# Kernel optimization log

Measured on AMD Instinct MI355X. Metric: run time of the kernel, lower is better.

Reference implementation:

```python
import jax, jax.numpy as jnp
import numpy as np

B, T, C = 4, 2048, 1024
N_HEAD = 16
HEAD_DIM = C // N_HEAD


def setup_inputs() -> dict:
    key = jax.random.key(0)
    k1, k2, k3 = jax.random.split(key, 3)
    x = jax.random.normal(k1, (B, T, C), dtype=jnp.float32)
    # torch Linear(n_embd, 3*n_embd, bias=False): weight [out,in]; store transposed [in,out]
    w_qkv = jax.random.normal(k2, (C, 3 * C), dtype=jnp.float32) * (1.0 / np.sqrt(C))
    w_proj = jax.random.normal(k3, (C, C), dtype=jnp.float32) * (1.0 / np.sqrt(C))
    return {"x": x, "w_qkv": w_qkv, "w_proj": w_proj}


def reference(x, w_qkv, w_proj):
    Bb, Tt, Cc = x.shape
    qkv = x @ w_qkv  # [B,T,3C]
    q, k, v = jnp.split(qkv, 3, axis=2)
    # [B,T,H,D] -> [B,H,T,D]
    def heads(t):
        return t.reshape(Bb, Tt, N_HEAD, HEAD_DIM).transpose(0, 2, 1, 3)
    q, k, v = heads(q), heads(k), heads(v)
    att = jnp.einsum("bhqd,bhkd->bhqk", q, k) / jnp.sqrt(jnp.float32(HEAD_DIM))
    causal = jnp.tril(jnp.ones((Tt, Tt), dtype=bool))
    att = jnp.where(causal, att, -jnp.inf)
    att = jax.nn.softmax(att, axis=-1)
    y = jnp.einsum("bhqk,bhkd->bhqd", att, v)  # [B,H,T,D]
    y = y.transpose(0, 2, 1, 3).reshape(Bb, Tt, Cc)
    return y @ w_proj
```

## Files before the change

kernel.cpp:

```cpp
#include <hip/hip_runtime.h>
#include <hip/hip_bf16.h>

typedef unsigned short u16;
typedef __bf16 bf16x8 __attribute__((ext_vector_type(8)));
typedef float f32x4 __attribute__((ext_vector_type(4)));
typedef float f32x16 __attribute__((ext_vector_type(16)));
typedef unsigned short u16x8 __attribute__((ext_vector_type(8)));
typedef unsigned short u16x4 __attribute__((ext_vector_type(4)));
typedef unsigned int u32x4 __attribute__((ext_vector_type(4)));

__device__ __forceinline__ u16 f2bf(float f) {
  unsigned u = __builtin_bit_cast(unsigned, f);
  u += 0x7FFFu + ((u >> 16) & 1u);
  return (u16)(u >> 16);
}

__device__ __forceinline__ unsigned cvt_pk_bf16(float lo, float hi_) {
  unsigned r;
  asm("v_cvt_pk_bf16_f32 %0, %1, %2" : "=v"(r) : "v"(lo), "v"(hi_));
  return r;
}

#define GLD16(gp, lp)                                                          \
  __builtin_amdgcn_global_load_lds(                                            \
      (const __attribute__((address_space(1))) void*)(gp),                     \
      (__attribute__((address_space(3))) void*)(lp), 16, 0, 0)


__global__ __launch_bounds__(256) void cast_f32_bf16(
    const float* __restrict__ in, u16* __restrict__ out, int n4) {
  int i = blockIdx.x * 256 + threadIdx.x;
  if (i >= n4) return;
  float4 v = ((const float4*)in)[i];
  u16x4 o = {f2bf(v.x), f2bf(v.y), f2bf(v.z), f2bf(v.w)};
  *(u16x4*)(out + (size_t)i * 4) = o;
}

__global__ __launch_bounds__(256) void transpose_cast(
    const float* __restrict__ in, u16* __restrict__ out, int R, int C) {
  __shared__ float t[32][33];
  int c0 = blockIdx.x * 32, r0 = blockIdx.y * 32;
  int tx = threadIdx.x, ty = threadIdx.y;
#pragma unroll
  for (int k = 0; k < 4; ++k)
    t[ty + 8 * k][tx] = in[(size_t)(r0 + ty + 8 * k) * C + c0 + tx];
  __syncthreads();
#pragma unroll
  for (int k = 0; k < 4; ++k)
    out[(size_t)(c0 + ty + 8 * k) * R + r0 + tx] = f2bf(t[tx][ty + 8 * k]);
}


template <int EPI>
__global__ __launch_bounds__(256) void gemm_bt(
    const u16* __restrict__ A, const u16* __restrict__ Bt, int K,
    u16* __restrict__ Qd, u16* __restrict__ Kd, u16* __restrict__ Vd,
    float* __restrict__ Od, int N) {
  __shared__ u16 As[128 * 64];
  __shared__ u16 Bs[128 * 64];
  int tid = threadIdx.x;
  int l = tid & 63, w = tid >> 6;
  int wr = w >> 1, wc = w & 1;
  int lr = l & 15, lg = l >> 4;
  int m0 = blockIdx.y * 128, n0 = blockIdx.x * 128;

  f32x4 acc[4][4];
  f32x4 z4 = {0.f, 0.f, 0.f, 0.f};
#pragma unroll
  for (int mi = 0; mi < 4; ++mi)
#pragma unroll
    for (int ni = 0; ni < 4; ++ni) acc[mi][ni] = z4;

  for (int kt = 0; kt < K; kt += 64) {
#pragma unroll
    for (int it = 0; it < 4; ++it) {
      int q = it * 256 + tid;
      int r = q >> 3, s = q & 7;
      int sw = (s ^ (r & 7)) << 3;
      GLD16(A + (size_t)(m0 + r) * K + kt + sw, As + it * 2048 + w * 512);
      GLD16(Bt + (size_t)(n0 + r) * K + kt + sw, Bs + it * 2048 + w * 512);
    }
    __syncthreads();

#pragma unroll
    for (int ks2 = 0; ks2 < 2; ++ks2) {
      bf16x8 af[4], bfv[4];
#pragma unroll
      for (int mi = 0; mi < 4; ++mi) {
        int row = wr * 64 + mi * 16 + lr;
        af[mi] = *(const bf16x8*)&As[row * 64 + (((ks2 * 4 + lg) ^ (row & 7)) << 3)];
      }
#pragma unroll
      for (int ni = 0; ni < 4; ++ni) {
        int col = wc * 64 + ni * 16 + lr;
        bfv[ni] = *(const bf16x8*)&Bs[col * 64 + (((ks2 * 4 + lg) ^ (col & 7)) << 3)];
      }
#pragma unroll
      for (int mi = 0; mi < 4; ++mi)
#pragma unroll
        for (int ni = 0; ni < 4; ++ni)
          acc[mi][ni] = __builtin_amdgcn_mfma_f32_16x16x32_bf16(
              af[mi], bfv[ni], acc[mi][ni], 0, 0, 0);
    }
    __syncthreads();
  }

  if (EPI == 0) {
    int s_blk = n0 >> 10;
    u16* dst = (s_blk == 0) ? Qd : ((s_blk == 1) ? Kd : Vd);
#pragma unroll
    for (int mi = 0; mi < 4; ++mi)
#pragma unroll
      for (int ni = 0; ni < 4; ++ni)
#pragma unroll
        for (int i = 0; i < 4; ++i) {
          int m = m0 + wr * 64 + mi * 16 + lg * 4 + i;
          int n = n0 + wc * 64 + ni * 16 + lr;
          int b = m >> 11, t = m & 2047;
          int c = n & 1023, h = c >> 6, d = c & 63;
          dst[((size_t)(b * 16 + h) * 2048 + t) * 64 + d] = f2bf(acc[mi][ni][i]);
        }
  } else {
#pragma unroll
    for (int mi = 0; mi < 4; ++mi)
#pragma unroll
      for (int ni = 0; ni < 4; ++ni)
#pragma unroll
        for (int i = 0; i < 4; ++i) {
          int m = m0 + wr * 64 + mi * 16 + lg * 4 + i;
          int n = n0 + wc * 64 + ni * 16 + lr;
          Od[(size_t)m * N + n] = acc[mi][ni][i];
        }
  }
}


__global__ __launch_bounds__(256, 2) void attn_fwd(
    const u16* __restrict__ Qg, const u16* __restrict__ Kg,
    const u16* __restrict__ Vg, u16* __restrict__ Yg) {
  __shared__ u16 Ks[2][64 * 64];
  __shared__ u16 Vt[64 * 64];

  int tid = threadIdx.x;
  int l = tid & 63, w = tid >> 6;
  int l31 = l & 31, hi = l >> 5, l7 = l & 7;
  int bid = blockIdx.x;
  int pp = bid >> 6;
  int bh = bid & 63;
  const u16* Qb = Qg + (size_t)bh * 131072;
  const u16* Kb = Kg + (size_t)bh * 131072;
  const u16* Vb = Vg + (size_t)bh * 131072;
  int b = bh >> 4, h = bh & 15;

  int vtr = tid >> 3, vdq = tid & 7;

#pragma unroll 1
  for (int ph = 0; ph < 2; ++ph) {
    int qt = ph ? (15 - pp) : pp;
    int q0w = qt * 128 + w * 32;
    int jn = 2 * qt + 1;

    bf16x8 qreg[4];
#pragma unroll
    for (int ds = 0; ds < 4; ++ds)
      qreg[ds] =
          *(const bf16x8*)(Qb + (size_t)(q0w + l31) * 64 + ds * 16 + hi * 8);

    f32x16 o_acc[2];
#pragma unroll
    for (int dt = 0; dt < 2; ++dt)
#pragma unroll
      for (int r = 0; r < 16; ++r) o_acc[dt][r] = 0.f;
    float m_run = -3e38f, l_run = 0.f;

    u16x8 va, vb;
#pragma unroll
    for (int it = 0; it < 2; ++it) {
      int r = (it * 256 + tid) >> 3;
      GLD16(Kb + (size_t)r * 64 + (((tid & 7) ^ (r & 7)) << 3),
            &Ks[0][it * 2048 + w * 512]);
    }
    va = *(const u16x8*)(Vb + (size_t)(2 * vtr) * 64 + vdq * 8);
    vb = *(const u16x8*)(Vb + (size_t)(2 * vtr + 1) * 64 + vdq * 8);

    for (int j = 0; j <= jn; ++j) {
      int kv0 = j * 64;
      const u16* ksb = Ks[j & 1];
#pragma unroll
      for (int jj = 0; jj < 8; ++jj) {
        int d = vdq * 8 + jj;
        unsigned wv = (unsigned)va[jj] | ((unsigned)vb[jj] << 16);
        *(unsigned*)(Vt + d * 64 + (((vtr >> 2) ^ jj ^ vdq) << 3) +
                     ((vtr & 3) << 1)) = wv;
      }
      __syncthreads();

      if (j < jn) {
        int kv1 = kv0 + 64;
#pragma unroll
        for (int it = 0; it < 2; ++it) {
          int r = (it * 256 + tid) >> 3;
          GLD16(Kb + (size_t)(kv1 + r) * 64 + (((tid & 7) ^ (r & 7)) << 3),
                &Ks[(j + 1) & 1][it * 2048 + w * 512]);
        }
        va = *(const u16x8*)(Vb + (size_t)(kv1 + 2 * vtr) * 64 + vdq * 8);
        vb = *(const u16x8*)(Vb + (size_t)(kv1 + 2 * vtr + 1) * 64 + vdq * 8);
      }

      bool active = kv0 <= q0w + 31;
      if (active) {
        int qg = q0w + l31;
        bf16x8 kf[2][4];
#pragma unroll
        for (int kt = 0; kt < 2; ++kt)
#pragma unroll
          for (int ds = 0; ds < 4; ++ds)
            kf[kt][ds] = *(const bf16x8*)&ksb[(32 * kt + l31) * 64 +
                                              (((2 * ds + hi) ^ l7) << 3)];
        f32x16 sa[2];
        __builtin_amdgcn_s_setprio(1);
#pragma unroll
        for (int kt = 0; kt < 2; ++kt) {
          f32x16 acc;
#pragma unroll
          for (int r = 0; r < 16; ++r) acc[r] = 0.f;
#pragma unroll
          for (int ds = 0; ds < 4; ++ds)
            acc = __builtin_amdgcn_mfma_f32_32x32x16_bf16(kf[kt][ds], qreg[ds],
                                                          acc, 0, 0, 0);
          sa[kt] = acc;
        }
        __builtin_amdgcn_s_setprio(0);

        float mloc = -3e38f;
        if (kv0 + 63 > q0w) {
#pragma unroll
          for (int kt = 0; kt < 2; ++kt)
#pragma unroll
            for (int r = 0; r < 16; ++r) {
              int kg = kv0 + kt * 32 + ((r & 3) + 8 * (r >> 2) + 4 * hi);
              float v = sa[kt][r];
              v = (kg <= qg) ? v : -8e30f;
              sa[kt][r] = v;
              mloc = fmaxf(mloc, v);
            }
        } else {
#pragma unroll
          for (int kt = 0; kt < 2; ++kt)
#pragma unroll
            for (int r = 0; r < 16; ++r) mloc = fmaxf(mloc, sa[kt][r]);
        }
        float mx = fmaxf(mloc, __shfl_xor(mloc, 32)) * 0.125f;
        if (!__all(mx <= m_run + 8.f)) {
          float mn = fmaxf(m_run, mx);
          float fsc = __expf(m_run - mn);
          m_run = mn;
          l_run *= fsc;
#pragma unroll
          for (int r = 0; r < 16; ++r) {
            float fv = __shfl(fsc, (r & 3) + 8 * (r >> 2) + 4 * hi + 32 * hi);
            o_acc[0][r] *= fv;
            o_acc[1][r] *= fv;
          }
        }
        float mm = m_run * 1.44269504f;
        float lloc = 0.f;
#pragma unroll
        for (int kt = 0; kt < 2; ++kt)
#pragma unroll
          for (int r = 0; r < 16; ++r) {
            float p = exp2f(__builtin_fmaf(sa[kt][r], 0.18033688f, -mm));
            sa[kt][r] = p;
            lloc += p;
          }
        l_run += lloc + __shfl_xor(lloc, 32);
        unsigned pk0[8], pk1[8];
#pragma unroll
        for (int m = 0; m < 8; ++m) {
          pk0[m] = cvt_pk_bf16(sa[0][2 * m], sa[0][2 * m + 1]);
          pk1[m] = cvt_pk_bf16(sa[1][2 * m], sa[1][2 * m + 1]);
        }
        bf16x8 vf[2][4];
#pragma unroll
        for (int dt = 0; dt < 2; ++dt)
#pragma unroll
          for (int ks = 0; ks < 4; ++ks) {
            int d = 32 * dt + l31;
            int ch = ((2 * ks + hi) ^ (d & 7) ^ ((d >> 3) & 7)) & 7;
            vf[dt][ks] = *(const bf16x8*)&Vt[d * 64 + (ch << 3)];
          }
#pragma unroll
        for (int ks = 0; ks < 4; ++ks) {
          int c0 = 4 * (ks & 1);
          unsigned a0 = (ks < 2) ? pk0[c0] : pk1[c0];
          unsigned a1 = (ks < 2) ? pk0[c0 + 1] : pk1[c0 + 1];
          unsigned a2 = (ks < 2) ? pk0[c0 + 2] : pk1[c0 + 2];
          unsigned a3 = (ks < 2) ? pk0[c0 + 3] : pk1[c0 + 3];
          unsigned pubX = hi ? a0 : a2;
          unsigned pubY = hi ? a1 : a3;
          unsigned rx = (unsigned)__shfl_xor((int)pubX, 32);
          unsigned ry = (unsigned)__shfl_xor((int)pubY, 32);
          u32x4 fa;
          fa.x = hi ? rx : a0;
          fa.y = hi ? ry : a1;
          fa.z = hi ? a2 : rx;
          fa.w = hi ? a3 : ry;
          bf16x8 paf = __builtin_bit_cast(bf16x8, fa);
          __builtin_amdgcn_s_setprio(1);
#pragma unroll
          for (int dt = 0; dt < 2; ++dt)
            o_acc[dt] = __builtin_amdgcn_mfma_f32_32x32x16_bf16(
                paf, vf[dt][ks], o_acc[dt], 0, 0, 0);
          __builtin_amdgcn_s_setprio(0);
        }
      }
      __syncthreads();
    }

#pragma unroll
    for (int r = 0; r < 16; ++r) {
      int crow = (r & 3) + 8 * (r >> 2) + 4 * hi;
      float li = __shfl(l_run, crow + 32 * hi);
      float inv = 1.f / li;
      int q = q0w + crow;
#pragma unroll
      for (int dt = 0; dt < 2; ++dt) {
        float y = o_acc[dt][r] * inv;
        Yg[(size_t)(b * 2048 + q) * 1024 + h * 64 + dt * 32 + l31] = f2bf(y);
      }
    }
  }
}


extern "C" void kernel_launch(void* const* d_in, const int* in_sizes, int n_in,
                              void* d_out, int out_size, void* d_ws, size_t ws_size,
                              hipStream_t stream) {
  const float* x = (const float*)d_in[0];
  const float* w_qkv = (const float*)d_in[1];
  const float* w_proj = (const float*)d_in[2];
  float* out = (float*)d_out;
  u16* ws = (u16*)d_ws;

  u16* xb = ws;
  u16* wq = xb + 8388608;
  u16* wp = wq + 3145728;
  u16* Qb = wp + 1048576;
  u16* Kb = Qb + 8388608;
  u16* Vb = Kb + 8388608;
  u16* Yb = xb;

  cast_f32_bf16<<<8192, 256, 0, stream>>>(x, xb, 2097152);
  transpose_cast<<<dim3(96, 32), dim3(32, 8), 0, stream>>>(w_qkv, wq, 1024, 3072);
  transpose_cast<<<dim3(32, 32), dim3(32, 8), 0, stream>>>(w_proj, wp, 1024, 1024);
  gemm_bt<0><<<dim3(24, 64), 256, 0, stream>>>(xb, wq, 1024, Qb, Kb, Vb, nullptr, 3072);
  attn_fwd<<<512, 256, 0, stream>>>(Qb, Kb, Vb, Yb);
  gemm_bt<1><<<dim3(8, 64), 256, 0, stream>>>(Yb, wp, 1024, nullptr, nullptr, nullptr, out, 1024);
}
```

Before: 187.8 us.

## Split attention into 64-row query tiles with 128-thread blocks, heaviest first

The attention kernel changes from 512 blocks of 4 waves, each handling two paired 128-row query tiles, to 2048 blocks of 2 waves, each handling one 64-row query tile. Blocks are ordered so the longest causal tiles launch first, and the K/V staging loops are widened so two waves can fill the shared tiles. The aim is finer work granularity and better load balance across CUs. In exchange, each K/V tile is loaded once per 64 query rows instead of once per 128, which doubles K/V traffic, and there are more barriers per unit of work.

Result: faster. 180.5 us (-3.9%).

```diff
diff --git a/kernel.cpp b/kernel.cpp
--- a/kernel.cpp
+++ b/kernel.cpp
@@ -135,7 +135,7 @@
 }
 
 
-__global__ __launch_bounds__(256, 2) void attn_fwd(
+__global__ __launch_bounds__(128, 3) void attn_fwd(
     const u16* __restrict__ Qg, const u16* __restrict__ Kg,
     const u16* __restrict__ Vg, u16* __restrict__ Yg) {
   __shared__ u16 Ks[2][64 * 64];
@@ -145,189 +145,195 @@
   int l = tid & 63, w = tid >> 6;
   int l31 = l & 31, hi = l >> 5, l7 = l & 7;
   int bid = blockIdx.x;
-  int pp = bid >> 6;
+  int qt = 31 - (bid >> 6);
   int bh = bid & 63;
   const u16* Qb = Qg + (size_t)bh * 131072;
   const u16* Kb = Kg + (size_t)bh * 131072;
   const u16* Vb = Vg + (size_t)bh * 131072;
   int b = bh >> 4, h = bh & 15;
 
-  int vtr = tid >> 3, vdq = tid & 7;
-
-#pragma unroll 1
-  for (int ph = 0; ph < 2; ++ph) {
-    int qt = ph ? (15 - pp) : pp;
-    int q0w = qt * 128 + w * 32;
-    int jn = 2 * qt + 1;
-
-    bf16x8 qreg[4];
-#pragma unroll
-    for (int ds = 0; ds < 4; ++ds)
-      qreg[ds] =
-          *(const bf16x8*)(Qb + (size_t)(q0w + l31) * 64 + ds * 16 + hi * 8);
-
-    f32x16 o_acc[2];
-#pragma unroll
-    for (int dt = 0; dt < 2; ++dt)
-#pragma unroll
-      for (int r = 0; r < 16; ++r) o_acc[dt][r] = 0.f;
-    float m_run = -3e38f, l_run = 0.f;
-
-    u16x8 va, vb;
+  int t8 = tid >> 3, dq = tid & 7;
+  int q0w = qt * 64 + w * 32;
+  int jn = qt;
+
+  bf16x8 qreg[4];
+#pragma unroll
+  for (int ds = 0; ds < 4; ++ds)
+    qreg[ds] =
+        *(const bf16x8*)(Qb + (size_t)(q0w + l31) * 64 + ds * 16 + hi * 8);
+
+  f32x16 o_acc[2];
+#pragma unroll
+  for (int dt = 0; dt < 2; ++dt)
+#pragma unroll
+    for (int r = 0; r < 16; ++r) o_acc[dt][r] = 0.f;
+  float m_run = -3e38f, l_run = 0.f;
+
+  u16x8 va[2], vb[2];
+#pragma unroll
+  for (int it = 0; it < 4; ++it) {
+    int r = it * 16 + t8;
+    GLD16(Kb + (size_t)r * 64 + ((dq ^ (r & 7)) << 3),
+          &Ks[0][it * 1024 + w * 512]);
+  }
+#pragma unroll
+  for (int it = 0; it < 2; ++it) {
+    int rr = it * 16 + t8;
+    va[it] = *(const u16x8*)(Vb + (size_t)(2 * rr) * 64 + dq * 8);
+    vb[it] = *(const u16x8*)(Vb + (size_t)(2 * rr + 1) * 64 + dq * 8);
+  }
+
+  for (int j = 0; j <= jn; ++j) {
+    int kv0 = j * 64;
+    const u16* ksb = Ks[j & 1];
 #pragma unroll
     for (int it = 0; it < 2; ++it) {
-      int r = (it * 256 + tid) >> 3;
-      GLD16(Kb + (size_t)r * 64 + (((tid & 7) ^ (r & 7)) << 3),
-            &Ks[0][it * 2048 + w * 512]);
-    }
-    va = *(const u16x8*)(Vb + (size_t)(2 * vtr) * 64 + vdq * 8);
-    vb = *(const u16x8*)(Vb + (size_t)(2 * vtr + 1) * 64 + vdq * 8);
-
-    for (int j = 0; j <= jn; ++j) {
-      int kv0 = j * 64;
-      const u16* ksb = Ks[j & 1];
+      int rr = it * 16 + t8;
 #pragma unroll
       for (int jj = 0; jj < 8; ++jj) {
-        int d = vdq * 8 + jj;
-        unsigned wv = (unsigned)va[jj] | ((unsigned)vb[jj] << 16);
-        *(unsigned*)(Vt + d * 64 + (((vtr >> 2) ^ jj ^ vdq) << 3) +
-                     ((vtr & 3) << 1)) = wv;
-      }
-      __syncthreads();
-
-      if (j < jn) {
-        int kv1 = kv0 + 64;
-#pragma unroll
-        for (int it = 0; it < 2; ++it) {
-          int r = (it * 256 + tid) >> 3;
-          GLD16(Kb + (size_t)(kv1 + r) * 64 + (((tid & 7) ^ (r & 7)) << 3),
-                &Ks[(j + 1) & 1][it * 2048 + w * 512]);
-        }
-        va = *(const u16x8*)(Vb + (size_t)(kv1 + 2 * vtr) * 64 + vdq * 8);
-        vb = *(const u16x8*)(Vb + (size_t)(kv1 + 2 * vtr + 1) * 64 + vdq * 8);
-      }
-
-      bool active = kv0 <= q0w + 31;
-      if (active) {
-        int qg = q0w + l31;
-        bf16x8 kf[2][4];
+        int d = dq * 8 + jj;
+        unsigned wv = (unsigned)va[it][jj] | ((unsigned)vb[it][jj] << 16);
+        *(unsigned*)(Vt + d * 64 + (((rr >> 2) ^ jj ^ dq) << 3) +
+                     ((rr & 3) << 1)) = wv;
+      }
+    }
+    __syncthreads();
+
+    if (j < jn) {
+      int kv1 = kv0 + 64;
+#pragma unroll
+      for (int it = 0; it < 4; ++it) {
+        int r = it * 16 + t8;
+        GLD16(Kb + (size_t)(kv1 + r) * 64 + ((dq ^ (r & 7)) << 3),
+              &Ks[(j + 1) & 1][it * 1024 + w * 512]);
+      }
+#pragma unroll
+      for (int it = 0; it < 2; ++it) {
+        int rr = it * 16 + t8;
+        va[it] = *(const u16x8*)(Vb + (size_t)(kv1 + 2 * rr) * 64 + dq * 8);
+        vb[it] = *(const u16x8*)(Vb + (size_t)(kv1 + 2 * rr + 1) * 64 + dq * 8);
+      }
+    }
+
+    {
+      int qg = q0w + l31;
+      bf16x8 kf[2][4];
+#pragma unroll
+      for (int kt = 0; kt < 2; ++kt)
+#pragma unroll
+        for (int ds = 0; ds < 4; ++ds)
+          kf[kt][ds] = *(const bf16x8*)&ksb[(32 * kt + l31) * 64 +
+                                            (((2 * ds + hi) ^ l7) << 3)];
+      f32x16 sa[2];
+      __builtin_amdgcn_s_setprio(1);
+#pragma unroll
+      for (int kt = 0; kt < 2; ++kt) {
+        f32x16 acc;
+#pragma unroll
+        for (int r = 0; r < 16; ++r) acc[r] = 0.f;
+#pragma unroll
+        for (int ds = 0; ds < 4; ++ds)
+          acc = __builtin_amdgcn_mfma_f32_32x32x16_bf16(kf[kt][ds], qreg[ds],
+                                                        acc, 0, 0, 0);
+        sa[kt] = acc;
+      }
+      __builtin_amdgcn_s_setprio(0);
+
+      float mloc = -3e38f;
+      if (kv0 + 63 > q0w) {
 #pragma unroll
         for (int kt = 0; kt < 2; ++kt)
 #pragma unroll
-          for (int ds = 0; ds < 4; ++ds)
-            kf[kt][ds] = *(const bf16x8*)&ksb[(32 * kt + l31) * 64 +
-                                              (((2 * ds + hi) ^ l7) << 3)];
-        f32x16 sa[2];
+          for (int r = 0; r < 16; ++r) {
+            int kg = kv0 + kt * 32 + ((r & 3) + 8 * (r >> 2) + 4 * hi);
+            float v = sa[kt][r];
+            v = (kg <= qg) ? v : -8e30f;
+            sa[kt][r] = v;
+            mloc = fmaxf(mloc, v);
+          }
+      } else {
+#pragma unroll
+        for (int kt = 0; kt < 2; ++kt)
+#pragma unroll
+          for (int r = 0; r < 16; ++r) mloc = fmaxf(mloc, sa[kt][r]);
+      }
+      float mx = fmaxf(mloc, __shfl_xor(mloc, 32)) * 0.125f;
+      if (!__all(mx <= m_run + 8.f)) {
+        float mn = fmaxf(m_run, mx);
+        float fsc = __expf(m_run - mn);
+        m_run = mn;
+        l_run *= fsc;
+#pragma unroll
+        for (int r = 0; r < 16; ++r) {
+          float fv = __shfl(fsc, (r & 3) + 8 * (r >> 2) + 4 * hi + 32 * hi);
+          o_acc[0][r] *= fv;
+          o_acc[1][r] *= fv;
+        }
+      }
+      float mm = m_run * 1.44269504f;
+      float lloc = 0.f;
+#pragma unroll
+      for (int kt = 0; kt < 2; ++kt)
+#pragma unroll
+        for (int r = 0; r < 16; ++r) {
+          float p = exp2f(__builtin_fmaf(sa[kt][r], 0.18033688f, -mm));
+          sa[kt][r] = p;
+          lloc += p;
+        }
+      l_run += lloc + __shfl_xor(lloc, 32);
+      unsigned pk0[8], pk1[8];
+#pragma unroll
+      for (int m = 0; m < 8; ++m) {
+        pk0[m] = cvt_pk_bf16(sa[0][2 * m], sa[0][2 * m + 1]);
+        pk1[m] = cvt_pk_bf16(sa[1][2 * m], sa[1][2 * m + 1]);
+      }
+      bf16x8 vf[2][4];
+#pragma unroll
+      for (int dt = 0; dt < 2; ++dt)
+#pragma unroll
+        for (int ks = 0; ks < 4; ++ks) {
+          int d = 32 * dt + l31;
+          int ch = ((2 * ks + hi) ^ (d & 7) ^ ((d >> 3) & 7)) & 7;
+          vf[dt][ks] = *(const bf16x8*)&Vt[d * 64 + (ch << 3)];
+        }
+#pragma unroll
+      for (int ks = 0; ks < 4; ++ks) {
+        int c0 = 4 * (ks & 1);
+        unsigned a0 = (ks < 2) ? pk0[c0] : pk1[c0];
+        unsigned a1 = (ks < 2) ? pk0[c0 + 1] : pk1[c0 + 1];
+        unsigned a2 = (ks < 2) ? pk0[c0 + 2] : pk1[c0 + 2];
+        unsigned a3 = (ks < 2) ? pk0[c0 + 3] : pk1[c0 + 3];
+        unsigned pubX = hi ? a0 : a2;
+        unsigned pubY = hi ? a1 : a3;
+        unsigned rx = (unsigned)__shfl_xor((int)pubX, 32);
+        unsigned ry = (unsigned)__shfl_xor((int)pubY, 32);
+        u32x4 fa;
+        fa.x = hi ? rx : a0;
+        fa.y = hi ? ry : a1;
+        fa.z = hi ? a2 : rx;
+        fa.w = hi ? a3 : ry;
+        bf16x8 paf = __builtin_bit_cast(bf16x8, fa);
         __builtin_amdgcn_s_setprio(1);
 #pragma unroll
-        for (int kt = 0; kt < 2; ++kt) {
-          f32x16 acc;
-#pragma unroll
-          for (int r = 0; r < 16; ++r) acc[r] = 0.f;
-#pragma unroll
-          for (int ds = 0; ds < 4; ++ds)
-            acc = __builtin_amdgcn_mfma_f32_32x32x16_bf16(kf[kt][ds], qreg[ds],
-                                                          acc, 0, 0, 0);
-          sa[kt] = acc;
-        }
+        for (int dt = 0; dt < 2; ++dt)
+          o_acc[dt] = __builtin_amdgcn_mfma_f32_32x32x16_bf16(
+              paf, vf[dt][ks], o_acc[dt], 0, 0, 0);
         __builtin_amdgcn_s_setprio(0);
-
-        float mloc = -3e38f;
-        if (kv0 + 63 > q0w) {
-#pragma unroll
-          for (int kt = 0; kt < 2; ++kt)
-#pragma unroll
-            for (int r = 0; r < 16; ++r) {
-              int kg = kv0 + kt * 32 + ((r & 3) + 8 * (r >> 2) + 4 * hi);
-              float v = sa[kt][r];
-              v = (kg <= qg) ? v : -8e30f;
-              sa[kt][r] = v;
-              mloc = fmaxf(mloc, v);
-            }
-        } else {
-#pragma unroll
-          for (int kt = 0; kt < 2; ++kt)
-#pragma unroll
-            for (int r = 0; r < 16; ++r) mloc = fmaxf(mloc, sa[kt][r]);
-        }
-        float mx = fmaxf(mloc, __shfl_xor(mloc, 32)) * 0.125f;
-        if (!__all(mx <= m_run + 8.f)) {
-          float mn = fmaxf(m_run, mx);
-          float fsc = __expf(m_run - mn);
-          m_run = mn;
-          l_run *= fsc;
-#pragma unroll
-          for (int r = 0; r < 16; ++r) {
-            float fv = __shfl(fsc, (r & 3) + 8 * (r >> 2) + 4 * hi + 32 * hi);
-            o_acc[0][r] *= fv;
-            o_acc[1][r] *= fv;
-          }
-        }
-        float mm = m_run * 1.44269504f;
-        float lloc = 0.f;
-#pragma unroll
-        for (int kt = 0; kt < 2; ++kt)
-#pragma unroll
-          for (int r = 0; r < 16; ++r) {
-            float p = exp2f(__builtin_fmaf(sa[kt][r], 0.18033688f, -mm));
-            sa[kt][r] = p;
-            lloc += p;
-          }
-        l_run += lloc + __shfl_xor(lloc, 32);
-        unsigned pk0[8], pk1[8];
-#pragma unroll
-        for (int m = 0; m < 8; ++m) {
-          pk0[m] = cvt_pk_bf16(sa[0][2 * m], sa[0][2 * m + 1]);
-          pk1[m] = cvt_pk_bf16(sa[1][2 * m], sa[1][2 * m + 1]);
-        }
-        bf16x8 vf[2][4];
-#pragma unroll
-        for (int dt = 0; dt < 2; ++dt)
-#pragma unroll
-          for (int ks = 0; ks < 4; ++ks) {
-            int d = 32 * dt + l31;
-            int ch = ((2 * ks + hi) ^ (d & 7) ^ ((d >> 3) & 7)) & 7;
-            vf[dt][ks] = *(const bf16x8*)&Vt[d * 64 + (ch << 3)];
-          }
-#pragma unroll
-        for (int ks = 0; ks < 4; ++ks) {
-          int c0 = 4 * (ks & 1);
-          unsigned a0 = (ks < 2) ? pk0[c0] : pk1[c0];
-          unsigned a1 = (ks < 2) ? pk0[c0 + 1] : pk1[c0 + 1];
-          unsigned a2 = (ks < 2) ? pk0[c0 + 2] : pk1[c0 + 2];
-          unsigned a3 = (ks < 2) ? pk0[c0 + 3] : pk1[c0 + 3];
-          unsigned pubX = hi ? a0 : a2;
-          unsigned pubY = hi ? a1 : a3;
-          unsigned rx = (unsigned)__shfl_xor((int)pubX, 32);
-          unsigned ry = (unsigned)__shfl_xor((int)pubY, 32);
-          u32x4 fa;
-          fa.x = hi ? rx : a0;
-          fa.y = hi ? ry : a1;
-          fa.z = hi ? a2 : rx;
-          fa.w = hi ? a3 : ry;
-          bf16x8 paf = __builtin_bit_cast(bf16x8, fa);
-          __builtin_amdgcn_s_setprio(1);
-#pragma unroll
-          for (int dt = 0; dt < 2; ++dt)
-            o_acc[dt] = __builtin_amdgcn_mfma_f32_32x32x16_bf16(
-                paf, vf[dt][ks], o_acc[dt], 0, 0, 0);
-          __builtin_amdgcn_s_setprio(0);
-        }
-      }
-      __syncthreads();
-    }
-
-#pragma unroll
-    for (int r = 0; r < 16; ++r) {
-      int crow = (r & 3) + 8 * (r >> 2) + 4 * hi;
-      float li = __shfl(l_run, crow + 32 * hi);
-      float inv = 1.f / li;
-      int q = q0w + crow;
-#pragma unroll
-      for (int dt = 0; dt < 2; ++dt) {
-        float y = o_acc[dt][r] * inv;
-        Yg[(size_t)(b * 2048 + q) * 1024 + h * 64 + dt * 32 + l31] = f2bf(y);
-      }
+      }
+    }
+    __syncthreads();
+  }
+
+#pragma unroll
+  for (int r = 0; r < 16; ++r) {
+    int crow = (r & 3) + 8 * (r >> 2) + 4 * hi;
+    float li = __shfl(l_run, crow + 32 * hi);
+    float inv = 1.f / li;
+    int q = q0w + crow;
+#pragma unroll
+    for (int dt = 0; dt < 2; ++dt) {
+      float y = o_acc[dt][r] * inv;
+      Yg[(size_t)(b * 2048 + q) * 1024 + h * 64 + dt * 32 + l31] = f2bf(y);
     }
   }
 }
@@ -354,6 +360,6 @@
   transpose_cast<<<dim3(96, 32), dim3(32, 8), 0, stream>>>(w_qkv, wq, 1024, 3072);
   transpose_cast<<<dim3(32, 32), dim3(32, 8), 0, stream>>>(w_proj, wp, 1024, 1024);
   gemm_bt<0><<<dim3(24, 64), 256, 0, stream>>>(xb, wq, 1024, Qb, Kb, Vb, nullptr, 3072);
-  attn_fwd<<<512, 256, 0, stream>>>(Qb, Kb, Vb, Yb);
+  attn_fwd<<<2048, 128, 0, stream>>>(Qb, Kb, Vb, Yb);
   gemm_bt<1><<<dim3(8, 64), 256, 0, stream>>>(Yb, wp, 1024, nullptr, nullptr, nullptr, out, 1024);
 }
```
